# Performance work log

Measured on AMD Instinct MI355X. Metric: run time of the kernel, lower is better.

## Reference

```python
import jax, jax.numpy as jnp
import numpy as np

N_NODES = 100000
N_EDGES = 1600000
DIMS = [(2, 128), (128, 128), (128, 32), (32, 32), (32, 32)]


def setup_inputs() -> dict:
    key = jax.random.key(0)
    ks = jax.random.split(key, 2 + 3 * len(DIMS) + 2)
    x = jax.random.normal(ks[0], (N_NODES, 2), dtype=jnp.float32)
    edge_index = jax.random.randint(ks[1], (2, N_EDGES), 0, N_NODES, dtype=jnp.int32)
    inp = {"x": x, "edge_index": edge_index, "batch_size": 100}
    k = 2
    for i, (cin, cout) in enumerate(DIMS, start=1):
        s = 1.0 / np.sqrt(cin)
        inp[f"Wl{i}"] = jax.random.normal(ks[k], (cin, cout), dtype=jnp.float32) * s; k += 1
        inp[f"bl{i}"] = jnp.zeros((cout,), dtype=jnp.float32)
        inp[f"Wr{i}"] = jax.random.normal(ks[k], (cin, cout), dtype=jnp.float32) * s; k += 1
    inp["W_out"] = jax.random.normal(ks[k], (32, 1), dtype=jnp.float32) * (1.0 / np.sqrt(32.0)); k += 1
    inp["b_out"] = jnp.zeros((1,), dtype=jnp.float32)
    return inp


def reference(x, edge_index, batch_size,
              Wl1, bl1, Wr1, Wl2, bl2, Wr2, Wl3, bl3, Wr3,
              Wl4, bl4, Wr4, Wl5, bl5, Wr5, W_out, b_out):
    src, dst = edge_index[0], edge_index[1]
    h = x.reshape(-1, 2)
    n = h.shape[0]
    # in-degree per target node, clamped to 1 (PyG mean aggr gives 0 for isolated nodes)
    deg = jax.ops.segment_sum(jnp.ones_like(src, dtype=h.dtype), dst, num_segments=n)
    inv_deg = (1.0 / jnp.maximum(deg, 1.0))[:, None]

    def sage(h, Wl, bl, Wr):
        # mean-aggregate neighbor features, then SAGEConv: lin_l(agg) + lin_r(h)
        agg = jax.ops.segment_sum(h[src], dst, num_segments=n) * inv_deg
        return agg @ Wl + bl + h @ Wr

    for Wl, bl, Wr in ((Wl1, bl1, Wr1), (Wl2, bl2, Wr2), (Wl3, bl3, Wr3),
                       (Wl4, bl4, Wr4), (Wl5, bl5, Wr5)):
        h = jax.nn.relu(sage(h, Wl, bl, Wr))
    # dropout is identity in eval mode
    out = h @ W_out + b_out  # [n, 1]
    return out.reshape(batch_size, -1)
```

## Files before the change

kernel.cpp:

```cpp
#include <hip/hip_runtime.h>
#include <hip/hip_bf16.h>

#define N_NODES 100000
#define N_EDGES 1600000
#define NBUCK 256
#define NODES_PER_BUCKET 391
#define EDGES_PER_CHUNK (N_EDGES / NBUCK)
#define FILL_LDS_CAP 8192

typedef __bf16 bf16x8 __attribute__((ext_vector_type(8)));
typedef float f32x4 __attribute__((ext_vector_type(4)));


__device__ inline unsigned short f2bf_rne(float v) {
    unsigned u = __float_as_uint(v);
    u += 0x7fffu + ((u >> 16) & 1u);
    return (unsigned short)(u >> 16);
}

__device__ inline unsigned pack_bf(float a, float b) {
    return (unsigned)f2bf_rne(a) | ((unsigned)f2bf_rne(b) << 16);
}

__device__ inline void acc8_bf(float* a, uint4 p) {
    a[0] += __uint_as_float(p.x << 16);
    a[1] += __uint_as_float(p.x & 0xffff0000u);
    a[2] += __uint_as_float(p.y << 16);
    a[3] += __uint_as_float(p.y & 0xffff0000u);
    a[4] += __uint_as_float(p.z << 16);
    a[5] += __uint_as_float(p.z & 0xffff0000u);
    a[6] += __uint_as_float(p.w << 16);
    a[7] += __uint_as_float(p.w & 0xffff0000u);
}


__global__ __launch_bounds__(256) void pa_count(const int* __restrict__ dst,
                                                int* __restrict__ blkCntT) {
    __shared__ int hist[NBUCK];
    hist[threadIdx.x] = 0;
    __syncthreads();
    int b0 = blockIdx.x * EDGES_PER_CHUNK;
    int b1 = min(b0 + EDGES_PER_CHUNK, N_EDGES);
    for (int i = b0 + (int)threadIdx.x; i < b1; i += 256) {
        int d = __builtin_nontemporal_load(&dst[i]);
        atomicAdd(&hist[d / NODES_PER_BUCKET], 1);
    }
    __syncthreads();
    blkCntT[threadIdx.x * NBUCK + blockIdx.x] = hist[threadIdx.x];
}

__global__ __launch_bounds__(256) void pa_scan1(const int* __restrict__ blkCntT,
                                                int* __restrict__ blkBaseL,
                                                int* __restrict__ bucketTotal) {
    __shared__ int s[256];
    int t = threadIdx.x;
    int v = blkCntT[blockIdx.x * NBUCK + t];
    s[t] = v;
    __syncthreads();
    for (int off = 1; off < 256; off <<= 1) {
        int u = (t >= off) ? s[t - off] : 0;
        __syncthreads();
        s[t] += u;
        __syncthreads();
    }
    blkBaseL[blockIdx.x * NBUCK + t] = s[t] - v;
    if (t == 255) bucketTotal[blockIdx.x] = s[255];
}

__global__ __launch_bounds__(256) void pa_scan2(const int* __restrict__ bucketTotal,
                                                int* __restrict__ bstart,
                                                int* __restrict__ offsets) {
    __shared__ int s[256];
    int t = threadIdx.x;
    int v = bucketTotal[t];
    s[t] = v;
    __syncthreads();
    for (int off = 1; off < 256; off <<= 1) {
        int u = (t >= off) ? s[t - off] : 0;
        __syncthreads();
        s[t] += u;
        __syncthreads();
    }
    bstart[t] = s[t] - v;
    if (t == 255) {
        bstart[256] = s[255];
        offsets[N_NODES] = s[255];
    }
}

__global__ __launch_bounds__(256) void pa_scatter(const int* __restrict__ src,
                                                  const int* __restrict__ dst,
                                                  const int* __restrict__ blkCntT,
                                                  const int* __restrict__ blkBaseL,
                                                  const int* __restrict__ bstart,
                                                  int2* __restrict__ staging) {
    __shared__ int runStart[NBUCK];
    __shared__ int cur[NBUCK];
    __shared__ int gbase[NBUCK];
    __shared__ int2 buf[EDGES_PER_CHUNK];

    const int tid = threadIdx.x;
    const int g = blockIdx.x;
    const int b0 = g * EDGES_PER_CHUNK;
    const int b1 = min(b0 + EDGES_PER_CHUNK, N_EDGES);

    {
        __shared__ int s[256];
        int v = blkCntT[tid * NBUCK + g];
        s[tid] = v;
        __syncthreads();
        for (int off = 1; off < 256; off <<= 1) {
            int u = (tid >= off) ? s[tid - off] : 0;
            __syncthreads();
            s[tid] += u;
            __syncthreads();
        }
        runStart[tid] = s[tid] - v;
        cur[tid] = s[tid] - v;
        gbase[tid] = bstart[tid] + blkBaseL[tid * NBUCK + g];
    }
    __syncthreads();
    for (int i = b0 + tid; i < b1; i += 256) {
        int d = __builtin_nontemporal_load(&dst[i]);
        int s_ = __builtin_nontemporal_load(&src[i]);
        int k = d / NODES_PER_BUCKET;
        int p = atomicAdd(&cur[k], 1);
        buf[p] = make_int2(s_, d);
    }
    __syncthreads();
    int cnt = b1 - b0;
    for (int i = tid; i < cnt; i += 256) {
        int2 e = buf[i];
        int k = e.y / NODES_PER_BUCKET;
        staging[gbase[k] + (i - runStart[k])] = e;
    }
}

__global__ __launch_bounds__(512) void pc_fill(const int2* __restrict__ staging,
                                               const int* __restrict__ bstart,
                                               int* __restrict__ ssrc,
                                               int* __restrict__ offsets,
                                               float* __restrict__ inv_deg) {
    __shared__ int scnt[NODES_PER_BUCKET];
    __shared__ int sexc[NODES_PER_BUCKET];
    __shared__ int scur[NODES_PER_BUCKET];
    __shared__ int ssrcL[FILL_LDS_CAP];

    const int tid = threadIdx.x;
    const int b = blockIdx.x;
    const int node0 = b * NODES_PER_BUCKET;
    const int nn = min(node0 + NODES_PER_BUCKET, N_NODES) - node0;
    if (nn <= 0) return;
    const int es = bstart[b], ee = bstart[b + 1];
    const int cnt = ee - es;

    for (int j = tid; j < nn; j += 512) scnt[j] = 0;
    __syncthreads();
    for (int i = es + tid; i < ee; i += 512) {
        int2 e = staging[i];
        atomicAdd(&scnt[e.y - node0], 1);
    }
    __syncthreads();

    if (tid < 64) {
        int base = tid * 7;
        int vals[7];
        int run = 0;
#pragma unroll
        for (int j = 0; j < 7; ++j) {
            int idx = base + j;
            int c = (idx < nn) ? scnt[idx] : 0;
            vals[j] = run;
            run += c;
        }
        int inc = run;
#pragma unroll
        for (int off = 1; off < 64; off <<= 1) {
            int u = __shfl_up(inc, off, 64);
            if (tid >= off) inc += u;
        }
        int laneExcl = inc - run;
#pragma unroll
        for (int j = 0; j < 7; ++j) {
            int idx = base + j;
            if (idx < nn) sexc[idx] = laneExcl + vals[j];
        }
    }
    __syncthreads();

    for (int j = tid; j < nn; j += 512) {
        int c = scnt[j];
        int ex = sexc[j];
        offsets[node0 + j] = es + ex;
        inv_deg[node0 + j] = 1.0f / (float)max(c, 1);
        scur[j] = ex;
    }
    __syncthreads();

    if (cnt <= FILL_LDS_CAP) {
        for (int i = es + tid; i < ee; i += 512) {
            int2 e = staging[i];
            int p = atomicAdd(&scur[e.y - node0], 1);
            ssrcL[p] = e.x;
        }
        __syncthreads();
        for (int i = tid; i < cnt; i += 512) ssrc[es + i] = ssrcL[i];
    } else {
        for (int i = es + tid; i < ee; i += 512) {
            int2 e = staging[i];
            int p = atomicAdd(&scur[e.y - node0], 1);
            ssrc[es + p] = e.x;
        }
    }
}


__global__ __launch_bounds__(256) void aggregate_bf128(const unsigned short* __restrict__ hb,
                                                       const int* __restrict__ offs,
                                                       const int* __restrict__ ssrc,
                                                       const float* __restrict__ inv_deg,
                                                       unsigned short* __restrict__ aggb,
                                                       int nnodes) {
    int t = blockIdx.x * 256 + threadIdx.x;
    if (t >= nnodes * 16) return;
    int node = t >> 4;
    int c = t & 15;
    int b = offs[node], e = offs[node + 1];
    const uint4* __restrict__ hb4 = (const uint4*)hb;
    float acc[8] = {0.f, 0.f, 0.f, 0.f, 0.f, 0.f, 0.f, 0.f};
    int i = b;
    for (; i + 4 <= e; i += 4) {
        uint4 p0 = hb4[(size_t)ssrc[i] * 16 + c];
        uint4 p1 = hb4[(size_t)ssrc[i + 1] * 16 + c];
        uint4 p2 = hb4[(size_t)ssrc[i + 2] * 16 + c];
        uint4 p3 = hb4[(size_t)ssrc[i + 3] * 16 + c];
        acc8_bf(acc, p0);
        acc8_bf(acc, p1);
        acc8_bf(acc, p2);
        acc8_bf(acc, p3);
    }
    for (; i < e; ++i) {
        uint4 p = hb4[(size_t)ssrc[i] * 16 + c];
        acc8_bf(acc, p);
    }
    float s = inv_deg[node];
    uint4 o;
    o.x = pack_bf(acc[0] * s, acc[1] * s);
    o.y = pack_bf(acc[2] * s, acc[3] * s);
    o.z = pack_bf(acc[4] * s, acc[5] * s);
    o.w = pack_bf(acc[6] * s, acc[7] * s);
    ((uint4*)aggb)[t] = o;
}

__global__ __launch_bounds__(256) void aggregate_bf32(const unsigned short* __restrict__ hb,
                                                      const int* __restrict__ offs,
                                                      const int* __restrict__ ssrc,
                                                      const float* __restrict__ inv_deg,
                                                      float* __restrict__ agg, int nnodes) {
    int t = blockIdx.x * 256 + threadIdx.x;
    if (t >= nnodes * 4) return;
    int node = t >> 2;
    int c = t & 3;
    int b = offs[node], e = offs[node + 1];
    const uint4* __restrict__ hb4 = (const uint4*)hb;
    float acc[8] = {0.f, 0.f, 0.f, 0.f, 0.f, 0.f, 0.f, 0.f};
    int i = b;
    for (; i + 4 <= e; i += 4) {
        uint4 p0 = hb4[(size_t)ssrc[i] * 4 + c];
        uint4 p1 = hb4[(size_t)ssrc[i + 1] * 4 + c];
        uint4 p2 = hb4[(size_t)ssrc[i + 2] * 4 + c];
        uint4 p3 = hb4[(size_t)ssrc[i + 3] * 4 + c];
        acc8_bf(acc, p0);
        acc8_bf(acc, p1);
        acc8_bf(acc, p2);
        acc8_bf(acc, p3);
    }
    for (; i < e; ++i) {
        uint4 p = hb4[(size_t)ssrc[i] * 4 + c];
        acc8_bf(acc, p);
    }
    float s = inv_deg[node];
    float4* outp = (float4*)&agg[(size_t)node * 32 + c * 8];
    outp[0] = make_float4(acc[0] * s, acc[1] * s, acc[2] * s, acc[3] * s);
    outp[1] = make_float4(acc[4] * s, acc[5] * s, acc[6] * s, acc[7] * s);
}

__global__ __launch_bounds__(256) void aggregate2(const float* __restrict__ h,
                                                  const int* __restrict__ offs,
                                                  const int* __restrict__ ssrc,
                                                  const float* __restrict__ inv_deg,
                                                  float* __restrict__ agg, int nnodes) {
    int node = blockIdx.x * blockDim.x + threadIdx.x;
    if (node >= nnodes) return;
    int b = offs[node], e = offs[node + 1];
    const float2* __restrict__ h2 = (const float2*)h;
    float2 a0 = make_float2(0.f, 0.f), a1 = make_float2(0.f, 0.f);
    int i = b;
    for (; i + 2 <= e; i += 2) {
        float2 v = h2[ssrc[i]];
        float2 w = h2[ssrc[i + 1]];
        a0.x += v.x; a0.y += v.y;
        a1.x += w.x; a1.y += w.y;
    }
    if (i < e) {
        float2 v = h2[ssrc[i]];
        a0.x += v.x; a0.y += v.y;
    }
    float s = inv_deg[node];
    ((float2*)agg)[node] = make_float2((a0.x + a1.x) * s, (a0.y + a1.y) * s);
}


__global__ __launch_bounds__(256) void prep_wt(const float* __restrict__ Wl,
                                               const float* __restrict__ Wr,
                                               unsigned short* __restrict__ Wt) {
    int idx = blockIdx.x * 256 + threadIdx.x;
    int n = idx >> 8;
    int k = idx & 255;
    float v = (k < 128) ? Wl[k * 128 + n] : Wr[(k - 128) * 128 + n];
    Wt[idx] = f2bf_rne(v);
}

__global__ __launch_bounds__(256) void prep_w3(const float* __restrict__ Wl3,
                                               const float* __restrict__ Wr3,
                                               unsigned short* __restrict__ W3c) {
    int idx = blockIdx.x * 256 + threadIdx.x;
    if (idx >= 64 * 128) return;
    int n = idx >> 7;
    int k = idx & 127;
    float v = (n < 32) ? Wl3[k * 32 + n] : Wr3[k * 32 + (n - 32)];
    W3c[idx] = f2bf_rne(v);
}

__global__ __launch_bounds__(256) void prep_w32(const float* __restrict__ Wl,
                                                const float* __restrict__ Wr,
                                                unsigned short* __restrict__ Wc) {
    int idx = blockIdx.x * 256 + threadIdx.x;
    if (idx >= 64 * 32) return;
    int n = idx >> 5;
    int k = idx & 31;
    float v = (n < 32) ? Wl[k * 32 + n] : Wr[k * 32 + (n - 32)];
    Wc[idx] = f2bf_rne(v);
}


__global__ __launch_bounds__(256) void gemm_l2_mfma(const unsigned short* __restrict__ Ab,
                                                    const unsigned short* __restrict__ Hb,
                                                    const unsigned short* __restrict__ Wt,
                                                    const float* __restrict__ bias,
                                                    const unsigned short* __restrict__ W3c,
                                                    unsigned short* __restrict__ g3b,
                                                    float* __restrict__ p3, int M) {
    constexpr int BM = 128, BK = 64;
    __shared__ unsigned short smem[26112];
#define SA(r, c) smem[(r) * 72 + (c)]
#define SB(r, c) smem[9216 + (r) * 72 + (c)]
#define SH(r, c) smem[(r) * 136 + (c)]
#define SW3(r, c) smem[17408 + (r) * 136 + (c)]

    const int tid = threadIdx.x;
    const int m0 = blockIdx.x * BM;
    const int lane = tid & 63;
    const int wid = tid >> 6;
    const int l15 = lane & 15;
    const int quad = lane >> 4;
    const int wm = (wid >> 1) * 64;
    const int wn = (wid & 1) * 64;

    f32x4 acc[4][4];
#pragma unroll
    for (int i = 0; i < 4; ++i)
#pragma unroll
        for (int j = 0; j < 4; ++j) acc[i][j] = (f32x4){0.f, 0.f, 0.f, 0.f};

    for (int k0 = 0; k0 < 256; k0 += BK) {
        const uint4* __restrict__ srcA = (const uint4*)((k0 < 128) ? Ab : Hb);
        const int kc = (k0 & 64) >> 3;
#pragma unroll
        for (int l = 0; l < 4; ++l) {
            int idx = tid + l * 256;
            int row = idx >> 3;
            int c8 = idx & 7;
            int gr = min(m0 + row, M - 1);
            uint4 va = srcA[(size_t)gr * 16 + kc + c8];
            *(uint4*)&SA(row, c8 * 8) = va;
            uint4 vb = ((const uint4*)Wt)[(size_t)row * 32 + (k0 >> 3) + c8];
            *(uint4*)&SB(row, c8 * 8) = vb;
        }
        __syncthreads();

#pragma unroll
        for (int ks = 0; ks < BK; ks += 32) {
            bf16x8 a[4], b[4];
#pragma unroll
            for (int t = 0; t < 4; ++t) {
                a[t] = *(const bf16x8*)&SA(wm + t * 16 + l15, ks + quad * 8);
                b[t] = *(const bf16x8*)&SB(wn + t * 16 + l15, ks + quad * 8);
            }
#pragma unroll
            for (int i = 0; i < 4; ++i)
#pragma unroll
                for (int j = 0; j < 4; ++j)
                    acc[i][j] = __builtin_amdgcn_mfma_f32_16x16x32_bf16(
                        a[i], b[j], acc[i][j], 0, 0, 0);
        }
        __syncthreads();
    }

#pragma unroll
    for (int j = 0; j < 4; ++j) {
        int n = wn + j * 16 + l15;
        float bv = bias[n];
#pragma unroll
        for (int i = 0; i < 4; ++i) {
#pragma unroll
            for (int r = 0; r < 4; ++r) {
                int ml = wm + i * 16 + quad * 4 + r;
                SH(ml, n) = f2bf_rne(fmaxf(acc[i][j][r] + bv, 0.f));
            }
        }
    }
#pragma unroll
    for (int l = 0; l < 4; ++l) {
        int idx = tid + l * 256;
        int row = idx >> 4;
        int c8 = idx & 15;
        uint4 v = ((const uint4*)W3c)[(size_t)row * 16 + c8];
        *(uint4*)&SW3(row, c8 * 8) = v;
    }
    __syncthreads();

    f32x4 acc2[2][4];
#pragma unroll
    for (int i = 0; i < 2; ++i)
#pragma unroll
        for (int j = 0; j < 4; ++j) acc2[i][j] = (f32x4){0.f, 0.f, 0.f, 0.f};

#pragma unroll
    for (int ks = 0; ks < 128; ks += 32) {
        bf16x8 a[2], b[4];
#pragma unroll
        for (int i = 0; i < 2; ++i)
            a[i] = *(const bf16x8*)&SH(wid * 32 + i * 16 + l15, ks + quad * 8);
#pragma unroll
        for (int j = 0; j < 4; ++j)
            b[j] = *(const bf16x8*)&SW3(j * 16 + l15, ks + quad * 8);
#pragma unroll
        for (int i = 0; i < 2; ++i)
#pragma unroll
            for (int j = 0; j < 4; ++j)
                acc2[i][j] = __builtin_amdgcn_mfma_f32_16x16x32_bf16(
                    a[i], b[j], acc2[i][j], 0, 0, 0);
    }

#pragma unroll
    for (int i = 0; i < 2; ++i) {
#pragma unroll
        for (int r = 0; r < 4; ++r) {
            int m = m0 + wid * 32 + i * 16 + quad * 4 + r;
            if (m >= M) continue;
#pragma unroll
            for (int j = 0; j < 4; ++j) {
                float v = acc2[i][j][r];
                if (j < 2) g3b[(size_t)m * 32 + j * 16 + l15] = f2bf_rne(v);
                else       p3[(size_t)m * 32 + (j - 2) * 16 + l15] = v;
            }
        }
    }
#undef SA
#undef SB
#undef SH
#undef SW3
}


__global__ __launch_bounds__(256) void combine_mfma(const float* __restrict__ agg,
                                                    const float* __restrict__ p,
                                                    const float* __restrict__ bias,
                                                    const unsigned short* __restrict__ Wc,
                                                    unsigned short* __restrict__ gb,
                                                    float* __restrict__ pnext, int M) {
    __shared__ unsigned short sH[128][40];
    __shared__ unsigned short sW[64][40];

    const int tid = threadIdx.x;
    const int m0 = blockIdx.x * 128;
    const int lane = tid & 63;
    const int wid = tid >> 6;
    const int l15 = lane & 15;
    const int quad = lane >> 4;

#pragma unroll
    for (int l = 0; l < 4; ++l) {
        int idx = tid + l * 256;
        int row = idx >> 3;
        int c4 = idx & 7;
        int gr = min(m0 + row, M - 1);
        float4 a = *(const float4*)&agg[(size_t)gr * 32 + c4 * 4];
        float4 pv = *(const float4*)&p[(size_t)gr * 32 + c4 * 4];
        float4 bv = *(const float4*)&bias[c4 * 4];
        uint2 o;
        o.x = pack_bf(fmaxf(a.x + pv.x + bv.x, 0.f), fmaxf(a.y + pv.y + bv.y, 0.f));
        o.y = pack_bf(fmaxf(a.z + pv.z + bv.z, 0.f), fmaxf(a.w + pv.w + bv.w, 0.f));
        *(uint2*)&sH[row][c4 * 4] = o;
    }
#pragma unroll
    for (int l = 0; l < 2; ++l) {
        int idx = tid + l * 256;
        int row = idx >> 3;
        int c4 = idx & 7;
        uint2 v = ((const uint2*)Wc)[(size_t)row * 8 + c4];
        *(uint2*)&sW[row][c4 * 4] = v;
    }
    __syncthreads();

    f32x4 acc[2][4];
    bf16x8 a[2], b[4];
#pragma unroll
    for (int i = 0; i < 2; ++i)
        a[i] = *(const bf16x8*)&sH[wid * 32 + i * 16 + l15][quad * 8];
#pragma unroll
    for (int j = 0; j < 4; ++j)
        b[j] = *(const bf16x8*)&sW[j * 16 + l15][quad * 8];
#pragma unroll
    for (int i = 0; i < 2; ++i)
#pragma unroll
        for (int j = 0; j < 4; ++j)
            acc[i][j] = __builtin_amdgcn_mfma_f32_16x16x32_bf16(
                a[i], b[j], (f32x4){0.f, 0.f, 0.f, 0.f}, 0, 0, 0);

#pragma unroll
    for (int i = 0; i < 2; ++i) {
#pragma unroll
        for (int r = 0; r < 4; ++r) {
            int m = m0 + wid * 32 + i * 16 + quad * 4 + r;
            if (m >= M) continue;
#pragma unroll
            for (int j = 0; j < 4; ++j) {
                float v = acc[i][j][r];
                if (j < 2) gb[(size_t)m * 32 + j * 16 + l15] = f2bf_rne(v);
                else       pnext[(size_t)m * 32 + (j - 2) * 16 + l15] = v;
            }
        }
    }
}

__global__ __launch_bounds__(256) void final5(const float* __restrict__ agg,
                                              const float* __restrict__ p,
                                              const float* __restrict__ bias,
                                              const float* __restrict__ Wout,
                                              const float* __restrict__ bout,
                                              float* __restrict__ out, int nnodes) {
    int n = blockIdx.x * 256 + threadIdx.x;
    if (n >= nnodes) return;
    const float4* a4 = (const float4*)(agg + (size_t)n * 32);
    const float4* p4 = (const float4*)(p + (size_t)n * 32);
    float acc = bout[0];
#pragma unroll
    for (int k4 = 0; k4 < 8; ++k4) {
        float4 a = a4[k4];
        float4 pv = p4[k4];
        const float* bv = bias + k4 * 4;
        const float* w = Wout + k4 * 4;
        acc = fmaf(fmaxf(a.x + pv.x + bv[0], 0.f), w[0], acc);
        acc = fmaf(fmaxf(a.y + pv.y + bv[1], 0.f), w[1], acc);
        acc = fmaf(fmaxf(a.z + pv.z + bv[2], 0.f), w[2], acc);
        acc = fmaf(fmaxf(a.w + pv.w + bv[3], 0.f), w[3], acc);
    }
    out[n] = acc;
}

__global__ __launch_bounds__(256) void sage_linear2(const float* __restrict__ agg,
                                                    const float* __restrict__ h,
                                                    const float* __restrict__ Wl,
                                                    const float* __restrict__ bl,
                                                    const float* __restrict__ Wr,
                                                    unsigned short* __restrict__ out_bf,
                                                    int nnodes) {
    constexpr int Cout = 128;
    int t = blockIdx.x * blockDim.x + threadIdx.x;
    if (t >= nnodes * Cout) return;
    int node = t / Cout;
    int c = t - node * Cout;
    float2 a = ((const float2*)agg)[node];
    float2 hh = ((const float2*)h)[node];
    float acc = bl[c];
    acc = fmaf(a.x, Wl[c], acc);
    acc = fmaf(a.y, Wl[Cout + c], acc);
    acc = fmaf(hh.x, Wr[c], acc);
    acc = fmaf(hh.y, Wr[Cout + c], acc);
    acc = fmaxf(acc, 0.f);
    out_bf[t] = f2bf_rne(acc);
}


extern "C" void kernel_launch(void* const* d_in, const int* in_sizes, int n_in,
                              void* d_out, int out_size, void* d_ws, size_t ws_size,
                              hipStream_t stream) {
    const float* x      = (const float*)d_in[0];
    const int*   ei     = (const int*)d_in[1];
    const float* Wl1    = (const float*)d_in[3];
    const float* bl1    = (const float*)d_in[4];
    const float* Wr1    = (const float*)d_in[5];
    const float* Wl2    = (const float*)d_in[6];
    const float* bl2    = (const float*)d_in[7];
    const float* Wr2    = (const float*)d_in[8];
    const float* Wl3    = (const float*)d_in[9];
    const float* bl3    = (const float*)d_in[10];
    const float* Wr3    = (const float*)d_in[11];
    const float* Wl4    = (const float*)d_in[12];
    const float* bl4    = (const float*)d_in[13];
    const float* Wr4    = (const float*)d_in[14];
    const float* Wl5    = (const float*)d_in[15];
    const float* bl5    = (const float*)d_in[16];
    const float* Wr5    = (const float*)d_in[17];
    const float* W_out  = (const float*)d_in[18];
    const float* b_out  = (const float*)d_in[19];
    float* out = (float*)d_out;

    const int N = N_NODES, E = N_EDGES;
    const int* e_src = ei;
    const int* e_dst = ei + E;

    size_t off = 0;
    auto carve = [&](size_t bytes) {
        void* p = (char*)d_ws + off;
        off += (bytes + 255) & ~(size_t)255;
        return p;
    };
    int*   offsets  = (int*)carve((size_t)(N + 1) * 4);
    float* inv_deg  = (float*)carve((size_t)N * 4);
    int*   ssrc     = (int*)carve((size_t)E * 4);
    int*   blkCntT  = (int*)carve((size_t)NBUCK * NBUCK * 4);
    int*   blkBaseL = (int*)carve((size_t)NBUCK * NBUCK * 4);
    int*   bucketTotal = (int*)carve((size_t)NBUCK * 4);
    int*   bstart   = (int*)carve((size_t)(NBUCK + 1) * 4);
    int2*  staging  = (int2*)carve((size_t)E * 8);
    unsigned short* Wt  = (unsigned short*)carve((size_t)128 * 256 * 2);
    unsigned short* W3c = (unsigned short*)carve((size_t)64 * 128 * 2);
    unsigned short* W4c = (unsigned short*)carve((size_t)64 * 32 * 2);
    unsigned short* W5c = (unsigned short*)carve((size_t)64 * 32 * 2);
    float* agg      = (float*)carve((size_t)N * 128 * 4);
    float* bufA     = (float*)carve((size_t)N * 128 * 4);
    unsigned short* g3b = (unsigned short*)carve((size_t)N * 32 * 2);
    unsigned short* g4b = (unsigned short*)carve((size_t)N * 32 * 2);
    unsigned short* g5b = (unsigned short*)carve((size_t)N * 32 * 2);

    float* slotA = agg;
    float* slotB = agg + (size_t)N * 32;
    float* slotC = agg + (size_t)N * 64;
    float* slotD = agg + (size_t)N * 96;
    unsigned short* h1_bf = (unsigned short*)bufA;
    unsigned short* aggB  = (unsigned short*)bufA + (size_t)N * 128;

    pa_count<<<NBUCK, 256, 0, stream>>>(e_dst, blkCntT);
    pa_scan1<<<NBUCK, 256, 0, stream>>>(blkCntT, blkBaseL, bucketTotal);
    pa_scan2<<<1, 256, 0, stream>>>(bucketTotal, bstart, offsets);
    pa_scatter<<<NBUCK, 256, 0, stream>>>(e_src, e_dst, blkCntT, blkBaseL, bstart, staging);
    pc_fill<<<NBUCK, 512, 0, stream>>>(staging, bstart, ssrc, offsets, inv_deg);
    prep_wt<<<128, 256, 0, stream>>>(Wl2, Wr2, Wt);
    prep_w3<<<32, 256, 0, stream>>>(Wl3, Wr3, W3c);
    prep_w32<<<8, 256, 0, stream>>>(Wl4, Wr4, W4c);
    prep_w32<<<8, 256, 0, stream>>>(Wl5, Wr5, W5c);

    const int gemm_grid = (N + 127) / 128;

    aggregate2<<<(N + 255) / 256, 256, 0, stream>>>(x, offsets, ssrc, inv_deg, slotC, N);
    sage_linear2<<<(N * 128 + 255) / 256, 256, 0, stream>>>(slotC, x, Wl1, bl1, Wr1, h1_bf, N);

    aggregate_bf128<<<(N * 16 + 255) / 256, 256, 0, stream>>>(h1_bf, offsets, ssrc,
                                                              inv_deg, aggB, N);
    gemm_l2_mfma<<<gemm_grid, 256, 0, stream>>>(aggB, h1_bf, Wt, bl2, W3c, g3b, slotA, N);

    aggregate_bf32<<<(N * 4 + 255) / 256, 256, 0, stream>>>(g3b, offsets, ssrc, inv_deg, slotB, N);
    combine_mfma<<<gemm_grid, 256, 0, stream>>>(slotB, slotA, bl3, W4c, g4b, slotC, N);

    aggregate_bf32<<<(N * 4 + 255) / 256, 256, 0, stream>>>(g4b, offsets, ssrc, inv_deg, slotD, N);
    combine_mfma<<<gemm_grid, 256, 0, stream>>>(slotD, slotC, bl4, W5c, g5b, slotA, N);

    aggregate_bf32<<<(N * 4 + 255) / 256, 256, 0, stream>>>(g5b, offsets, ssrc, inv_deg, slotB, N);
    final5<<<(N + 255) / 256, 256, 0, stream>>>(slotB, slotA, bl5, W_out, b_out, out, N);
}
```

Baseline: 372.5 us.

## Fuse 32-wide aggregation into combine MFMA and final output kernels

Merges each 32-channel neighbor aggregation with the following bias+ReLU+MFMA projection into a single kernel. Per-node aggregates stay in LDS instead of making an fp32 round trip through global memory. The final layer's aggregation is fused with the output dot product using a 4-lane shuffle reduction. The four weight-prep launches are combined into one kernel. This cuts launches and intermediate traffic, at the cost of smaller 64-node blocks and a __syncthreads after gather latency.

```diff
diff --git a/kernel.cpp b/kernel.cpp
--- a/kernel.cpp
+++ b/kernel.cpp
@@ -252,39 +252,6 @@
     ((uint4*)aggb)[t] = o;
 }
 
-__global__ __launch_bounds__(256) void aggregate_bf32(const unsigned short* __restrict__ hb,
-                                                      const int* __restrict__ offs,
-                                                      const int* __restrict__ ssrc,
-                                                      const float* __restrict__ inv_deg,
-                                                      float* __restrict__ agg, int nnodes) {
-    int t = blockIdx.x * 256 + threadIdx.x;
-    if (t >= nnodes * 4) return;
-    int node = t >> 2;
-    int c = t & 3;
-    int b = offs[node], e = offs[node + 1];
-    const uint4* __restrict__ hb4 = (const uint4*)hb;
-    float acc[8] = {0.f, 0.f, 0.f, 0.f, 0.f, 0.f, 0.f, 0.f};
-    int i = b;
-    for (; i + 4 <= e; i += 4) {
-        uint4 p0 = hb4[(size_t)ssrc[i] * 4 + c];
-        uint4 p1 = hb4[(size_t)ssrc[i + 1] * 4 + c];
-        uint4 p2 = hb4[(size_t)ssrc[i + 2] * 4 + c];
-        uint4 p3 = hb4[(size_t)ssrc[i + 3] * 4 + c];
-        acc8_bf(acc, p0);
-        acc8_bf(acc, p1);
-        acc8_bf(acc, p2);
-        acc8_bf(acc, p3);
-    }
-    for (; i < e; ++i) {
-        uint4 p = hb4[(size_t)ssrc[i] * 4 + c];
-        acc8_bf(acc, p);
-    }
-    float s = inv_deg[node];
-    float4* outp = (float4*)&agg[(size_t)node * 32 + c * 8];
-    outp[0] = make_float4(acc[0] * s, acc[1] * s, acc[2] * s, acc[3] * s);
-    outp[1] = make_float4(acc[4] * s, acc[5] * s, acc[6] * s, acc[7] * s);
-}
-
 __global__ __launch_bounds__(256) void aggregate2(const float* __restrict__ h,
                                                   const int* __restrict__ offs,
                                                   const int* __restrict__ ssrc,
@@ -311,36 +278,39 @@
 }
 
 
-__global__ __launch_bounds__(256) void prep_wt(const float* __restrict__ Wl,
-                                               const float* __restrict__ Wr,
-                                               unsigned short* __restrict__ Wt) {
+__global__ __launch_bounds__(256) void prep_all(const float* __restrict__ Wl2,
+                                                const float* __restrict__ Wr2,
+                                                const float* __restrict__ Wl3,
+                                                const float* __restrict__ Wr3,
+                                                const float* __restrict__ Wl4,
+                                                const float* __restrict__ Wr4,
+                                                const float* __restrict__ Wl5,
+                                                const float* __restrict__ Wr5,
+                                                unsigned short* __restrict__ Wt,
+                                                unsigned short* __restrict__ W3c,
+                                                unsigned short* __restrict__ W4c,
+                                                unsigned short* __restrict__ W5c) {
     int idx = blockIdx.x * 256 + threadIdx.x;
-    int n = idx >> 8;
-    int k = idx & 255;
-    float v = (k < 128) ? Wl[k * 128 + n] : Wr[(k - 128) * 128 + n];
-    Wt[idx] = f2bf_rne(v);
-}
-
-__global__ __launch_bounds__(256) void prep_w3(const float* __restrict__ Wl3,
-                                               const float* __restrict__ Wr3,
-                                               unsigned short* __restrict__ W3c) {
-    int idx = blockIdx.x * 256 + threadIdx.x;
-    if (idx >= 64 * 128) return;
-    int n = idx >> 7;
-    int k = idx & 127;
-    float v = (n < 32) ? Wl3[k * 32 + n] : Wr3[k * 32 + (n - 32)];
-    W3c[idx] = f2bf_rne(v);
-}
-
-__global__ __launch_bounds__(256) void prep_w32(const float* __restrict__ Wl,
-                                                const float* __restrict__ Wr,
-                                                unsigned short* __restrict__ Wc) {
-    int idx = blockIdx.x * 256 + threadIdx.x;
-    if (idx >= 64 * 32) return;
-    int n = idx >> 5;
-    int k = idx & 31;
-    float v = (n < 32) ? Wl[k * 32 + n] : Wr[k * 32 + (n - 32)];
-    Wc[idx] = f2bf_rne(v);
+    if (idx < 32768) {
+        int n = idx >> 8, k = idx & 255;
+        float v = (k < 128) ? Wl2[k * 128 + n] : Wr2[(k - 128) * 128 + n];
+        Wt[idx] = f2bf_rne(v);
+    } else if (idx < 32768 + 8192) {
+        int j = idx - 32768;
+        int n = j >> 7, k = j & 127;
+        float v = (n < 32) ? Wl3[k * 32 + n] : Wr3[k * 32 + (n - 32)];
+        W3c[j] = f2bf_rne(v);
+    } else if (idx < 32768 + 8192 + 2048) {
+        int j = idx - 32768 - 8192;
+        int n = j >> 5, k = j & 31;
+        float v = (n < 32) ? Wl4[k * 32 + n] : Wr4[k * 32 + (n - 32)];
+        W4c[j] = f2bf_rne(v);
+    } else if (idx < 32768 + 8192 + 4096) {
+        int j = idx - 32768 - 8192 - 2048;
+        int n = j >> 5, k = j & 31;
+        float v = (n < 32) ? Wl5[k * 32 + n] : Wr5[k * 32 + (n - 32)];
+        W5c[j] = f2bf_rne(v);
+    }
 }
 
 
@@ -474,100 +444,143 @@
 }
 
 
-__global__ __launch_bounds__(256) void combine_mfma(const float* __restrict__ agg,
-                                                    const float* __restrict__ p,
-                                                    const float* __restrict__ bias,
-                                                    const unsigned short* __restrict__ Wc,
-                                                    unsigned short* __restrict__ gb,
-                                                    float* __restrict__ pnext, int M) {
-    __shared__ unsigned short sH[128][40];
-    __shared__ unsigned short sW[64][40];
+__global__ __launch_bounds__(256) void aggregate_combine32(
+        const unsigned short* __restrict__ gb_prev,
+        const int* __restrict__ offs,
+        const int* __restrict__ ssrc,
+        const float* __restrict__ inv_deg,
+        const float* __restrict__ p,
+        const float* __restrict__ bias,
+        const unsigned short* __restrict__ Wc,
+        unsigned short* __restrict__ g_next,
+        float* __restrict__ p_next, int nnodes) {
+    __shared__ unsigned short hB[64][40];
+    __shared__ unsigned short wB[64][40];
 
     const int tid = threadIdx.x;
-    const int m0 = blockIdx.x * 128;
+    const int node0 = blockIdx.x * 64;
+    const int node = node0 + (tid >> 2);
+    const int c = tid & 3;
+    const int ln = tid >> 2;
+
+#pragma unroll
+    for (int l = 0; l < 2; ++l) {
+        int id = tid + l * 256;
+        int r = id >> 3, cc = id & 7;
+        uint2 v = ((const uint2*)Wc)[(size_t)r * 8 + cc];
+        *(uint2*)&wB[r][cc * 4] = v;
+    }
+
+    uint4 hout = make_uint4(0u, 0u, 0u, 0u);
+    if (node < nnodes) {
+        int b = offs[node], e = offs[node + 1];
+        const uint4* __restrict__ hb4 = (const uint4*)gb_prev;
+        float acc[8] = {0.f, 0.f, 0.f, 0.f, 0.f, 0.f, 0.f, 0.f};
+        int i = b;
+        for (; i + 4 <= e; i += 4) {
+            uint4 p0 = hb4[(size_t)ssrc[i] * 4 + c];
+            uint4 p1 = hb4[(size_t)ssrc[i + 1] * 4 + c];
+            uint4 p2 = hb4[(size_t)ssrc[i + 2] * 4 + c];
+            uint4 p3 = hb4[(size_t)ssrc[i + 3] * 4 + c];
+            acc8_bf(acc, p0);
+            acc8_bf(acc, p1);
+            acc8_bf(acc, p2);
+            acc8_bf(acc, p3);
+        }
+        for (; i < e; ++i) acc8_bf(acc, hb4[(size_t)ssrc[i] * 4 + c]);
+        float s = inv_deg[node];
+        const float4* prow = (const float4*)(p + (size_t)node * 32 + c * 8);
+        float4 p0 = prow[0], p1 = prow[1];
+        const float* bb = bias + c * 8;
+        float h0 = fmaxf(acc[0] * s + p0.x + bb[0], 0.f);
+        float h1 = fmaxf(acc[1] * s + p0.y + bb[1], 0.f);
+        float h2 = fmaxf(acc[2] * s + p0.z + bb[2], 0.f);
+        float h3 = fmaxf(acc[3] * s + p0.w + bb[3], 0.f);
+        float h4 = fmaxf(acc[4] * s + p1.x + bb[4], 0.f);
+        float h5 = fmaxf(acc[5] * s + p1.y + bb[5], 0.f);
+        float h6 = fmaxf(acc[6] * s + p1.z + bb[6], 0.f);
+        float h7 = fmaxf(acc[7] * s + p1.w + bb[7], 0.f);
+        hout.x = pack_bf(h0, h1);
+        hout.y = pack_bf(h2, h3);
+        hout.z = pack_bf(h4, h5);
+        hout.w = pack_bf(h6, h7);
+    }
+    *(uint4*)&hB[ln][c * 8] = hout;
+    __syncthreads();
+
     const int lane = tid & 63;
     const int wid = tid >> 6;
     const int l15 = lane & 15;
     const int quad = lane >> 4;
 
-#pragma unroll
-    for (int l = 0; l < 4; ++l) {
-        int idx = tid + l * 256;
-        int row = idx >> 3;
-        int c4 = idx & 7;
-        int gr = min(m0 + row, M - 1);
-        float4 a = *(const float4*)&agg[(size_t)gr * 32 + c4 * 4];
-        float4 pv = *(const float4*)&p[(size_t)gr * 32 + c4 * 4];
-        float4 bv = *(const float4*)&bias[c4 * 4];
-        uint2 o;
-        o.x = pack_bf(fmaxf(a.x + pv.x + bv.x, 0.f), fmaxf(a.y + pv.y + bv.y, 0.f));
-        o.y = pack_bf(fmaxf(a.z + pv.z + bv.z, 0.f), fmaxf(a.w + pv.w + bv.w, 0.f));
-        *(uint2*)&sH[row][c4 * 4] = o;
-    }
-#pragma unroll
-    for (int l = 0; l < 2; ++l) {
-        int idx = tid + l * 256;
-        int row = idx >> 3;
-        int c4 = idx & 7;
-        uint2 v = ((const uint2*)Wc)[(size_t)row * 8 + c4];
-        *(uint2*)&sW[row][c4 * 4] = v;
-    }
-    __syncthreads();
-
-    f32x4 acc[2][4];
-    bf16x8 a[2], b[4];
-#pragma unroll
-    for (int i = 0; i < 2; ++i)
-        a[i] = *(const bf16x8*)&sH[wid * 32 + i * 16 + l15][quad * 8];
-#pragma unroll
-    for (int j = 0; j < 4; ++j)
-        b[j] = *(const bf16x8*)&sW[j * 16 + l15][quad * 8];
-#pragma unroll
-    for (int i = 0; i < 2; ++i)
-#pragma unroll
-        for (int j = 0; j < 4; ++j)
-            acc[i][j] = __builtin_amdgcn_mfma_f32_16x16x32_bf16(
-                a[i], b[j], (f32x4){0.f, 0.f, 0.f, 0.f}, 0, 0, 0);
-
-#pragma unroll
-    for (int i = 0; i < 2; ++i) {
-#pragma unroll
-        for (int r = 0; r < 4; ++r) {
-            int m = m0 + wid * 32 + i * 16 + quad * 4 + r;
-            if (m >= M) continue;
-#pragma unroll
-            for (int j = 0; j < 4; ++j) {
-                float v = acc[i][j][r];
-                if (j < 2) gb[(size_t)m * 32 + j * 16 + l15] = f2bf_rne(v);
-                else       pnext[(size_t)m * 32 + (j - 2) * 16 + l15] = v;
-            }
-        }
-    }
-}
-
-__global__ __launch_bounds__(256) void final5(const float* __restrict__ agg,
-                                              const float* __restrict__ p,
-                                              const float* __restrict__ bias,
-                                              const float* __restrict__ Wout,
-                                              const float* __restrict__ bout,
-                                              float* __restrict__ out, int nnodes) {
-    int n = blockIdx.x * 256 + threadIdx.x;
-    if (n >= nnodes) return;
-    const float4* a4 = (const float4*)(agg + (size_t)n * 32);
-    const float4* p4 = (const float4*)(p + (size_t)n * 32);
-    float acc = bout[0];
-#pragma unroll
-    for (int k4 = 0; k4 < 8; ++k4) {
-        float4 a = a4[k4];
-        float4 pv = p4[k4];
-        const float* bv = bias + k4 * 4;
-        const float* w = Wout + k4 * 4;
-        acc = fmaf(fmaxf(a.x + pv.x + bv[0], 0.f), w[0], acc);
-        acc = fmaf(fmaxf(a.y + pv.y + bv[1], 0.f), w[1], acc);
-        acc = fmaf(fmaxf(a.z + pv.z + bv[2], 0.f), w[2], acc);
-        acc = fmaf(fmaxf(a.w + pv.w + bv[3], 0.f), w[3], acc);
-    }
-    out[n] = acc;
+    bf16x8 a = *(const bf16x8*)&hB[wid * 16 + l15][quad * 8];
+    f32x4 accm[4];
+#pragma unroll
+    for (int j = 0; j < 4; ++j) {
+        bf16x8 b = *(const bf16x8*)&wB[j * 16 + l15][quad * 8];
+        accm[j] = __builtin_amdgcn_mfma_f32_16x16x32_bf16(
+            a, b, (f32x4){0.f, 0.f, 0.f, 0.f}, 0, 0, 0);
+    }
+
+#pragma unroll
+    for (int r = 0; r < 4; ++r) {
+        int m = node0 + wid * 16 + quad * 4 + r;
+        if (m >= nnodes) continue;
+#pragma unroll
+        for (int j = 0; j < 4; ++j) {
+            float v = accm[j][r];
+            if (j < 2) g_next[(size_t)m * 32 + j * 16 + l15] = f2bf_rne(v);
+            else       p_next[(size_t)m * 32 + (j - 2) * 16 + l15] = v;
+        }
+    }
+}
+
+__global__ __launch_bounds__(256) void aggregate_final32(
+        const unsigned short* __restrict__ gb_prev,
+        const int* __restrict__ offs,
+        const int* __restrict__ ssrc,
+        const float* __restrict__ inv_deg,
+        const float* __restrict__ p,
+        const float* __restrict__ bias,
+        const float* __restrict__ Wout,
+        const float* __restrict__ bout,
+        float* __restrict__ out, int nnodes) {
+    int t = blockIdx.x * 256 + threadIdx.x;
+    int node = t >> 2;
+    int c = t & 3;
+    if (node >= nnodes) return;
+    int b = offs[node], e = offs[node + 1];
+    const uint4* __restrict__ hb4 = (const uint4*)gb_prev;
+    float acc[8] = {0.f, 0.f, 0.f, 0.f, 0.f, 0.f, 0.f, 0.f};
+    int i = b;
+    for (; i + 4 <= e; i += 4) {
+        uint4 p0 = hb4[(size_t)ssrc[i] * 4 + c];
+        uint4 p1 = hb4[(size_t)ssrc[i + 1] * 4 + c];
+        uint4 p2 = hb4[(size_t)ssrc[i + 2] * 4 + c];
+        uint4 p3 = hb4[(size_t)ssrc[i + 3] * 4 + c];
+        acc8_bf(acc, p0);
+        acc8_bf(acc, p1);
+        acc8_bf(acc, p2);
+        acc8_bf(acc, p3);
+    }
+    for (; i < e; ++i) acc8_bf(acc, hb4[(size_t)ssrc[i] * 4 + c]);
+    float s = inv_deg[node];
+    const float4* prow = (const float4*)(p + (size_t)node * 32 + c * 8);
+    float4 p0 = prow[0], p1 = prow[1];
+    const float* bb = bias + c * 8;
+    const float* w = Wout + c * 8;
+    float sum = 0.f;
+    sum = fmaf(fmaxf(acc[0] * s + p0.x + bb[0], 0.f), w[0], sum);
+    sum = fmaf(fmaxf(acc[1] * s + p0.y + bb[1], 0.f), w[1], sum);
+    sum = fmaf(fmaxf(acc[2] * s + p0.z + bb[2], 0.f), w[2], sum);
+    sum = fmaf(fmaxf(acc[3] * s + p0.w + bb[3], 0.f), w[3], sum);
+    sum = fmaf(fmaxf(acc[4] * s + p1.x + bb[4], 0.f), w[4], sum);
+    sum = fmaf(fmaxf(acc[5] * s + p1.y + bb[5], 0.f), w[5], sum);
+    sum = fmaf(fmaxf(acc[6] * s + p1.z + bb[6], 0.f), w[6], sum);
+    sum = fmaf(fmaxf(acc[7] * s + p1.w + bb[7], 0.f), w[7], sum);
+    sum += __shfl_down(sum, 2, 4);
+    sum += __shfl_down(sum, 1, 4);
+    if (c == 0) out[node] = sum + bout[0];
 }
 
 __global__ __launch_bounds__(256) void sage_linear2(const float* __restrict__ agg,
@@ -647,9 +660,7 @@
     unsigned short* g5b = (unsigned short*)carve((size_t)N * 32 * 2);
 
     float* slotA = agg;
-    float* slotB = agg + (size_t)N * 32;
     float* slotC = agg + (size_t)N * 64;
-    float* slotD = agg + (size_t)N * 96;
     unsigned short* h1_bf = (unsigned short*)bufA;
     unsigned short* aggB  = (unsigned short*)bufA + (size_t)N * 128;
 
@@ -658,12 +669,11 @@
     pa_scan2<<<1, 256, 0, stream>>>(bucketTotal, bstart, offsets);
     pa_scatter<<<NBUCK, 256, 0, stream>>>(e_src, e_dst, blkCntT, blkBaseL, bstart, staging);
     pc_fill<<<NBUCK, 512, 0, stream>>>(staging, bstart, ssrc, offsets, inv_deg);
-    prep_wt<<<128, 256, 0, stream>>>(Wl2, Wr2, Wt);
-    prep_w3<<<32, 256, 0, stream>>>(Wl3, Wr3, W3c);
-    prep_w32<<<8, 256, 0, stream>>>(Wl4, Wr4, W4c);
-    prep_w32<<<8, 256, 0, stream>>>(Wl5, Wr5, W5c);
+    prep_all<<<176, 256, 0, stream>>>(Wl2, Wr2, Wl3, Wr3, Wl4, Wr4, Wl5, Wr5,
+                                      Wt, W3c, W4c, W5c);
 
     const int gemm_grid = (N + 127) / 128;
+    const int comb_grid = (N + 63) / 64;
 
     aggregate2<<<(N + 255) / 256, 256, 0, stream>>>(x, offsets, ssrc, inv_deg, slotC, N);
     sage_linear2<<<(N * 128 + 255) / 256, 256, 0, stream>>>(slotC, x, Wl1, bl1, Wr1, h1_bf, N);
@@ -672,12 +682,13 @@
                                                               inv_deg, aggB, N);
     gemm_l2_mfma<<<gemm_grid, 256, 0, stream>>>(aggB, h1_bf, Wt, bl2, W3c, g3b, slotA, N);
 
-    aggregate_bf32<<<(N * 4 + 255) / 256, 256, 0, stream>>>(g3b, offsets, ssrc, inv_deg, slotB, N);
-    combine_mfma<<<gemm_grid, 256, 0, stream>>>(slotB, slotA, bl3, W4c, g4b, slotC, N);
-
-    aggregate_bf32<<<(N * 4 + 255) / 256, 256, 0, stream>>>(g4b, offsets, ssrc, inv_deg, slotD, N);
-    combine_mfma<<<gemm_grid, 256, 0, stream>>>(slotD, slotC, bl4, W5c, g5b, slotA, N);
-
-    aggregate_bf32<<<(N * 4 + 255) / 256, 256, 0, stream>>>(g5b, offsets, ssrc, inv_deg, slotB, N);
-    final5<<<(N + 255) / 256, 256, 0, stream>>>(slotB, slotA, bl5, W_out, b_out, out, N);
-}
+    aggregate_combine32<<<comb_grid, 256, 0, stream>>>(g3b, offsets, ssrc, inv_deg,
+                                                       slotA, bl3, W4c, g4b, slotC, N);
+
+    aggregate_combine32<<<comb_grid, 256, 0, stream>>>(g4b, offsets, ssrc, inv_deg,
+                                                       slotC, bl4, W5c, g5b, slotA, N);
+
+    aggregate_final32<<<(N * 4 + 255) / 256, 256, 0, stream>>>(g5b, offsets, ssrc, inv_deg,
+                                                               slotA, bl5, W_out, b_out,
+                                                               out, N);
+}
```

After: 341.9 us. 8.2% less time.
